# Kernel optimization log

Measured on AMD Instinct MI355X. Metric: run time of the kernel, lower is better.

The kernel has to match this reference:

```python
import jax, jax.numpy as jnp
import numpy as np


def _log_g(x):
    # log of g(x) = where(x>=0, x+0.5, sigmoid(x)), computed stably in log-space
    return jnp.where(x >= 0, jnp.log(jax.nn.relu(x) + 0.5), -jax.nn.softplus(-x))


def _mingru_layer(h, w_hg_l, w_out_l, rms_w_l):
    # h: [B,T,H]; w_hg_l: [2*DI,H]; w_out_l: [H,DI]; rms_w_l: [H]
    hg = jnp.einsum('bth,dh->btd', h, w_hg_l)          # [B,T,2*DI]
    hidden, gate = jnp.split(hg, 2, axis=-1)            # each [B,T,DI]
    log_coeffs = -jax.nn.softplus(gate)                 # log a_t
    log_values = -jax.nn.softplus(-gate) + _log_g(hidden)  # log(z_t * g(h~_t))
    # Heinsen log-space associative scan (prev_hidden = 0, contributes nothing)
    a_star = jnp.cumsum(log_coeffs, axis=1)
    log_h = a_star + jax.lax.cumlogsumexp(log_values - a_star, axis=1)
    out = jnp.exp(log_h)                                # [B,T,DI]
    out = jnp.einsum('btd,hd->bth', out, w_out_l) + h   # proj_out + residual
    eps = jnp.finfo(out.dtype).eps
    out = out * jax.lax.rsqrt(jnp.mean(out * out, axis=-1, keepdims=True) + eps)
    return out * rms_w_l


def setup_inputs() -> dict:
    key = jax.random.key(0)
    ks = jax.random.split(key, 6)
    B, T, OBS, H, DI, L, A = 32, 1024, 512, 512, 1024, 2, 16
    s = 0.05  # weight scale keeps softplus/exp chain well-conditioned
    return {
        'x': jax.random.normal(ks[0], (B, T, OBS), jnp.float32),
        'enc_w': s * jax.random.normal(ks[1], (H, OBS), jnp.float32),
        'enc_b': jnp.zeros((H,), jnp.float32),
        'w_hg': s * jax.random.normal(ks[2], (L, 2 * DI, H), jnp.float32),
        'w_out': s * jax.random.normal(ks[3], (L, H, DI), jnp.float32),
        'rms_w': jnp.ones((L, H), jnp.float32),
        'dec_w': s * jax.random.normal(ks[4], (A, H), jnp.float32),
        'dec_b': jnp.zeros((A,), jnp.float32),
        'val_w': s * jax.random.normal(ks[5], (1, H), jnp.float32),
        'val_b': jnp.zeros((1,), jnp.float32),
    }


def reference(x, enc_w, enc_b, w_hg, w_out, rms_w, dec_w, dec_b, val_w, val_b):
    B, T, _ = x.shape
    # encoder: Linear + exact gelu
    h = jax.nn.gelu(jnp.einsum('bto,ho->bth', x, enc_w) + enc_b, approximate=False)
    for l in range(w_hg.shape[0]):
        h = _mingru_layer(h, w_hg[l], w_out[l], rms_w[l])
    flat = h.reshape(B * T, -1)
    logits = flat @ dec_w.T + dec_b                     # [B*T, A]
    values = (flat @ val_w.T + val_b).reshape(B, T)
    return logits, values
```

## Files before the change

kernel.cpp:

```cpp
#include <hip/hip_runtime.h>
#include <math.h>

#define MROWS 32768
#define T_LEN 1024

typedef __attribute__((ext_vector_type(8))) short bf16x8;
typedef __attribute__((ext_vector_type(4))) float f32x4;

__device__ __forceinline__ unsigned short f2bf(float f) {
  union { float f; unsigned u; } x; x.f = f;
  unsigned r = x.u + 0x7fffu + ((x.u >> 16) & 1u);
  return (unsigned short)(r >> 16);
}
__device__ __forceinline__ float bf2f(unsigned short u) {
  union { unsigned u; float f; } x; x.u = ((unsigned)u) << 16; return x.f;
}

__device__ __forceinline__ void gload_lds16(const void* g, void* l) {
  __builtin_amdgcn_global_load_lds(
      (const __attribute__((address_space(1))) void*)g,
      (__attribute__((address_space(3))) void*)l, 16, 0, 0);
}

__device__ __forceinline__ float sigm_neg(float x) {
  return __builtin_amdgcn_rcpf(1.0f + __expf(x));
}

template<int MODE>
__global__ __launch_bounds__(256, 2)
void gemm_bt(const unsigned short* __restrict__ A, int lda,
             const unsigned short* __restrict__ B,
             int N, int K,
             const float* __restrict__ bias,
             const unsigned short* res,
             unsigned short* outb)
{
  __shared__ __align__(16) unsigned short sA[128 * 64];
  __shared__ __align__(16) unsigned short sB[128 * 64];
  const int tid  = threadIdx.x;
  const int wave = tid >> 6, lane = tid & 63;
  const int lid = blockIdx.x;
  const int swz = (lid & 7) * ((int)gridDim.x >> 3) + (lid >> 3);
  const int m0 = (swz >> 2) * 128;
  const int n0 = (swz & 3) * 128;
  const int srow   = lane >> 3;
  const int sslotb = ((lane & 7) ^ srow) * 16;
  const int wm = wave & 1, wn = wave >> 1;
  const int r16 = lane & 15, q = lane >> 4;

  f32x4 acc[4][4];
#pragma unroll
  for (int i = 0; i < 4; i++)
#pragma unroll
    for (int j = 0; j < 4; j++)
#pragma unroll
      for (int e = 0; e < 4; e++) acc[i][j][e] = 0.0f;

  const char* Ab = (const char*)A;
  const char* Bb = (const char*)B;
  char* sAb = (char*)sA;
  char* sBb = (char*)sB;

  for (int kt = 0; kt < K; kt += 64) {
#pragma unroll
    for (int i = 0; i < 4; i++) {
      const int j = wave * 4 + i;
      const int row = j * 8 + srow;
      gload_lds16(Ab + ((size_t)(m0 + row) * lda + kt) * 2 + sslotb, sAb + j * 1024);
      gload_lds16(Bb + ((size_t)(n0 + row) * K   + kt) * 2 + sslotb, sBb + j * 1024);
    }
    __syncthreads();
#pragma unroll
    for (int kh = 0; kh < 2; kh++) {
      bf16x8 af[4], bfr[4];
#pragma unroll
      for (int mt = 0; mt < 4; mt++) {
        const int row = wm * 64 + mt * 16 + r16;
        af[mt] = *(const bf16x8*)(sAb + row * 128 + ((((kh << 2) | q) ^ (row & 7)) * 16));
      }
#pragma unroll
      for (int nt = 0; nt < 4; nt++) {
        const int row = wn * 64 + nt * 16 + r16;
        bfr[nt] = *(const bf16x8*)(sBb + row * 128 + ((((kh << 2) | q) ^ (row & 7)) * 16));
      }
#pragma unroll
      for (int mt = 0; mt < 4; mt++)
#pragma unroll
        for (int nt = 0; nt < 4; nt++)
          acc[mt][nt] = __builtin_amdgcn_mfma_f32_16x16x32_bf16(af[mt], bfr[nt], acc[mt][nt], 0, 0, 0);
    }
    __syncthreads();
  }

#pragma unroll
  for (int mt = 0; mt < 4; mt++) {
#pragma unroll
    for (int nt = 0; nt < 4; nt++) {
#pragma unroll
      for (int r = 0; r < 4; r++) {
        const int m = m0 + wm * 64 + mt * 16 + q * 4 + r;
        const int n = n0 + wn * 64 + nt * 16 + r16;
        const size_t idx = (size_t)m * N + n;
        float v = acc[mt][nt][r];
        if (MODE == 0) {
          v += bias[n];
          v = 0.5f * v * (1.0f + erff(v * 0.70710678118654752f));
        } else if (MODE == 2) {
          v += bf2f(res[idx]);
        }
        outb[idx] = f2bf(v);
      }
    }
  }
}

__global__ __launch_bounds__(256, 2)
void gemm_hg(const unsigned short* __restrict__ A,
             const unsigned short* __restrict__ B,
             unsigned short* __restrict__ outb)
{
  __shared__ __align__(16) unsigned short sA [128 * 64];
  __shared__ __align__(16) unsigned short sB0[128 * 64];
  __shared__ __align__(16) unsigned short sB1[128 * 64];
  const int tid  = threadIdx.x;
  const int wave = tid >> 6, lane = tid & 63;
  const int lid = blockIdx.x;
  const int swz = (lid & 7) * 256 + (lid >> 3);
  const int m0  = (swz >> 3) * 128;
  const int nh0 = (swz & 7) * 128;
  const int srow   = lane >> 3;
  const int sslotb = ((lane & 7) ^ srow) * 16;
  const int wm = wave & 1, wn = wave >> 1;
  const int r16 = lane & 15, q = lane >> 4;

  f32x4 acc0[4][4], acc1[4][4];
#pragma unroll
  for (int i = 0; i < 4; i++)
#pragma unroll
    for (int j = 0; j < 4; j++)
#pragma unroll
      for (int e = 0; e < 4; e++) { acc0[i][j][e] = 0.0f; acc1[i][j][e] = 0.0f; }

  const char* Ab = (const char*)A;
  const char* Bb = (const char*)B;
  char* sAb  = (char*)sA;
  char* sB0b = (char*)sB0;
  char* sB1b = (char*)sB1;

  for (int kt = 0; kt < 512; kt += 64) {
#pragma unroll
    for (int i = 0; i < 4; i++) {
      const int j = wave * 4 + i;
      const int row = j * 8 + srow;
      gload_lds16(Ab + ((size_t)(m0 + row) * 512 + kt) * 2 + sslotb, sAb + j * 1024);
      gload_lds16(Bb + ((size_t)(nh0 + row) * 512 + kt) * 2 + sslotb, sB0b + j * 1024);
      gload_lds16(Bb + ((size_t)(1024 + nh0 + row) * 512 + kt) * 2 + sslotb, sB1b + j * 1024);
    }
    __syncthreads();
#pragma unroll
    for (int kh = 0; kh < 2; kh++) {
      bf16x8 af[4], b0r[4], b1r[4];
#pragma unroll
      for (int mt = 0; mt < 4; mt++) {
        const int row = wm * 64 + mt * 16 + r16;
        af[mt] = *(const bf16x8*)(sAb + row * 128 + ((((kh << 2) | q) ^ (row & 7)) * 16));
      }
#pragma unroll
      for (int nt = 0; nt < 4; nt++) {
        const int row = wn * 64 + nt * 16 + r16;
        const int so  = ((((kh << 2) | q) ^ (row & 7)) * 16);
        b0r[nt] = *(const bf16x8*)(sB0b + row * 128 + so);
        b1r[nt] = *(const bf16x8*)(sB1b + row * 128 + so);
      }
#pragma unroll
      for (int mt = 0; mt < 4; mt++)
#pragma unroll
        for (int nt = 0; nt < 4; nt++) {
          acc0[mt][nt] = __builtin_amdgcn_mfma_f32_16x16x32_bf16(af[mt], b0r[nt], acc0[mt][nt], 0, 0, 0);
          acc1[mt][nt] = __builtin_amdgcn_mfma_f32_16x16x32_bf16(af[mt], b1r[nt], acc1[mt][nt], 0, 0, 0);
        }
    }
    __syncthreads();
  }

#pragma unroll
  for (int mt = 0; mt < 4; mt++) {
#pragma unroll
    for (int nt = 0; nt < 4; nt++) {
#pragma unroll
      for (int r = 0; r < 4; r++) {
        const int m  = m0 + wm * 64 + mt * 16 + q * 4 + r;
        const int d  = nh0 + wn * 64 + nt * 16 + r16;
        const float vh = acc0[mt][nt][r];
        const float vg = acc1[mt][nt][r];
        const float G = (vh >= 0.0f) ? (vh + 0.5f) : sigm_neg(-vh);
        const float a = sigm_neg(vg);
        const float b = (1.0f - a) * G;
        const size_t base = (size_t)m * 2048 + d;
        outb[base]        = f2bf(b);
        outb[base + 1024] = f2bf(a);
      }
    }
  }
}

__global__ __launch_bounds__(256)
void scan_kernel(unsigned short* hg) {
  __shared__ unsigned long long sAB[256 * 16];
  __shared__ float sA[16 * 32];
  __shared__ float sH[16 * 32];
  const int b  = blockIdx.x >> 5;
  const int dg = blockIdx.x & 31;
  const int tid = threadIdx.x;
  const int c  = tid >> 4;
  const int dp = tid & 15;
  unsigned int* base = (unsigned int*)(hg + (size_t)b * T_LEN * 2048);
  const int du = dg * 16 + dp;

  float carry = 0.0f;

  for (int seg = 0; seg < 4; ++seg) {
    const int t0 = seg * 256 + c * 16;

    float A0 = 1.0f, A1 = 1.0f, h0 = 0.0f, h1 = 0.0f;
#pragma unroll
    for (int tl = 0; tl < 16; ++tl) {
      const int t = t0 + tl;
      const unsigned bpk = base[t * 1024 + du];
      const unsigned apk = base[t * 1024 + 512 + du];
      sAB[(c * 16 + tl) * 16 + dp] =
          (unsigned long long)apk | ((unsigned long long)bpk << 32);
      const float fa0 = bf2f((unsigned short)apk), fa1 = bf2f((unsigned short)(apk >> 16));
      const float fb0 = bf2f((unsigned short)bpk), fb1 = bf2f((unsigned short)(bpk >> 16));
      A0 *= fa0; h0 = fa0 * h0 + fb0;
      A1 *= fa1; h1 = fa1 * h1 + fb1;
    }
    sA[c * 32 + 2 * dp] = A0;  sA[c * 32 + 2 * dp + 1] = A1;
    sH[c * 32 + 2 * dp] = h0;  sH[c * 32 + 2 * dp + 1] = h1;
    __syncthreads();

    if (tid < 32) {
      float hin = carry;
#pragma unroll
      for (int cc = 0; cc < 16; ++cc) {
        const float a  = sA[cc * 32 + tid];
        const float hs = sH[cc * 32 + tid];
        sA[cc * 32 + tid] = hin;
        hin = hs + a * hin;
      }
      carry = hin;
    }
    __syncthreads();

    float hh0 = sA[c * 32 + 2 * dp];
    float hh1 = sA[c * 32 + 2 * dp + 1];
#pragma unroll
    for (int tl = 0; tl < 16; ++tl) {
      const int t = t0 + tl;
      const unsigned long long ab = sAB[(c * 16 + tl) * 16 + dp];
      const float fa0 = bf2f((unsigned short)ab);
      const float fa1 = bf2f((unsigned short)(ab >> 16));
      const float fb0 = bf2f((unsigned short)(ab >> 32));
      const float fb1 = bf2f((unsigned short)(ab >> 48));
      hh0 = fa0 * hh0 + fb0;
      hh1 = fa1 * hh1 + fb1;
      base[t * 1024 + 512 + du] = (unsigned)f2bf(hh0) | ((unsigned)f2bf(hh1) << 16);
    }
    __syncthreads();
  }
}

__global__ __launch_bounds__(256)
void rms_kernel(unsigned short* __restrict__ hb, const float* __restrict__ w) {
  const int wid  = (blockIdx.x * blockDim.x + threadIdx.x) >> 6;
  const int lane = threadIdx.x & 63;
  unsigned short* row = hb + (size_t)wid * 512;
  float v[8];
  float ss = 0.0f;
#pragma unroll
  for (int j = 0; j < 8; j++) { v[j] = bf2f(row[lane + 64 * j]); ss += v[j] * v[j]; }
#pragma unroll
  for (int off = 32; off >= 1; off >>= 1) ss += __shfl_xor(ss, off, 64);
  const float r = rsqrtf(ss * (1.0f / 512.0f) + 1.1920929e-7f);
#pragma unroll
  for (int j = 0; j < 8; j++) {
    const int k = lane + 64 * j;
    row[k] = f2bf(v[j] * r * w[k]);
  }
}

__global__ __launch_bounds__(256)
void rms_dec_kernel(const unsigned short* __restrict__ hb,
                    const float* __restrict__ w,
                    const float* __restrict__ dec_w,
                    const float* __restrict__ dec_b,
                    const float* __restrict__ val_w,
                    const float* __restrict__ val_b,
                    float* __restrict__ out) {
  const int row  = (blockIdx.x * blockDim.x + threadIdx.x) >> 6;
  const int lane = threadIdx.x & 63;
  const unsigned short* hr = hb + (size_t)row * 512;
  float v[8];
  float ss = 0.0f;
#pragma unroll
  for (int j = 0; j < 8; j++) { v[j] = bf2f(hr[lane + 64 * j]); ss += v[j] * v[j]; }
#pragma unroll
  for (int off = 32; off >= 1; off >>= 1) ss += __shfl_xor(ss, off, 64);
  const float r = rsqrtf(ss * (1.0f / 512.0f) + 1.1920929e-7f);

  float acc[17];
#pragma unroll
  for (int a = 0; a < 17; a++) acc[a] = 0.0f;
#pragma unroll
  for (int j = 0; j < 8; j++) {
    const int k = lane + 64 * j;
    const float hv = v[j] * r * w[k];
#pragma unroll
    for (int a = 0; a < 16; a++) acc[a] += hv * dec_w[a * 512 + k];
    acc[16] += hv * val_w[k];
  }
#pragma unroll
  for (int a = 0; a < 17; a++) {
#pragma unroll
    for (int off = 32; off >= 1; off >>= 1) acc[a] += __shfl_xor(acc[a], off, 64);
  }
  if (lane == 0) {
    float* logits = out;
    float* values = out + (size_t)MROWS * 16;
#pragma unroll
    for (int a = 0; a < 16; a++) logits[(size_t)row * 16 + a] = acc[a] + dec_b[a];
    values[row] = acc[16] + val_b[0];
  }
}

__global__ __launch_bounds__(256)
void conv_bf16(const float* __restrict__ in, unsigned short* __restrict__ out, int n4) {
  const int i = blockIdx.x * blockDim.x + threadIdx.x;
  if (i < n4) {
    const float4 v = ((const float4*)in)[i];
    const unsigned long long pack =
        (unsigned long long)f2bf(v.x) |
        ((unsigned long long)f2bf(v.y) << 16) |
        ((unsigned long long)f2bf(v.z) << 32) |
        ((unsigned long long)f2bf(v.w) << 48);
    ((unsigned long long*)out)[i] = pack;
  }
}

extern "C" void kernel_launch(void* const* d_in, const int* in_sizes, int n_in,
                              void* d_out, int out_size, void* d_ws, size_t ws_size,
                              hipStream_t stream) {
  const float* x     = (const float*)d_in[0];
  const float* enc_w = (const float*)d_in[1];
  const float* enc_b = (const float*)d_in[2];
  const float* w_hg  = (const float*)d_in[3];
  const float* w_out = (const float*)d_in[4];
  const float* rms_w = (const float*)d_in[5];
  const float* dec_w = (const float*)d_in[6];
  const float* dec_b = (const float*)d_in[7];
  const float* val_w = (const float*)d_in[8];
  const float* val_b = (const float*)d_in[9];
  float* out = (float*)d_out;

  if (ws_size < 174587904u) return;

  char* ws = (char*)d_ws;
  unsigned short* hg   = (unsigned short*)(ws);
  unsigned short* xb   = (unsigned short*)(ws);
  unsigned short* hb   = (unsigned short*)(ws + 134217728);
  unsigned short* wenc = (unsigned short*)(ws + 167772160);
  unsigned short* whg  = wenc + 262144;
  unsigned short* wout = whg + 2097152;

  conv_bf16<<<16384, 256, 0, stream>>>(x, xb, 4194304);
  conv_bf16<<<256,   256, 0, stream>>>(enc_w, wenc, 65536);
  conv_bf16<<<2048,  256, 0, stream>>>(w_hg, whg, 524288);
  conv_bf16<<<1024,  256, 0, stream>>>(w_out, wout, 262144);

  gemm_bt<0><<<1024, 256, 0, stream>>>(xb, 512, wenc, 512, 512, enc_b, nullptr, hb);

  for (int l = 0; l < 2; ++l) {
    gemm_hg<<<2048, 256, 0, stream>>>(hb, whg + (size_t)l * 1048576, hg);
    scan_kernel<<<1024, 256, 0, stream>>>(hg);
    gemm_bt<2><<<1024, 256, 0, stream>>>(hg + 1024, 2048, wout + (size_t)l * 524288,
                                         512, 1024, nullptr, hb, hb);
    if (l == 0) rms_kernel<<<8192, 256, 0, stream>>>(hb, rms_w);
  }

  rms_dec_kernel<<<8192, 256, 0, stream>>>(hb, rms_w + 512, dec_w, dec_b,
                                           val_w, val_b, out);
}
```

Baseline: 603.8 us.

## Rewrite hidden/gate GEMM with 256-row tiles and double-buffered async LDS pipeline

Replaces the 128x(2x128) hidden/gate GEMM with an 8-wave, 256-row tile kernel that uses a 128 KB double-buffered LDS ring. It streams the next K-step's global-to-LDS loads in quarters while computing on the current buffer, using explicit vmcnt/lgkmcnt waits, barriers and MFMA priority boosts. The aim is to hide global load latency and raise reuse of the weight tile per block. The cost is heavy LDS use (128 KB) and delicate hand-written synchronisation.

```diff
diff --git a/kernel.cpp b/kernel.cpp
--- a/kernel.cpp
+++ b/kernel.cpp
@@ -25,6 +25,12 @@
 __device__ __forceinline__ float sigm_neg(float x) {
   return __builtin_amdgcn_rcpf(1.0f + __expf(x));
 }
+
+#define VMCNT2 asm volatile("s_waitcnt vmcnt(2)" ::: "memory")
+#define VMCNT0 asm volatile("s_waitcnt vmcnt(0)" ::: "memory")
+#define LGKM0 do { asm volatile("s_waitcnt lgkmcnt(0)" ::: "memory"); \
+                   __builtin_amdgcn_sched_barrier(0); } while (0)
+#define BAR __builtin_amdgcn_s_barrier()
 
 template<int MODE>
 __global__ __launch_bounds__(256, 2)
@@ -114,85 +120,144 @@
   }
 }
 
-__global__ __launch_bounds__(256, 2)
-void gemm_hg(const unsigned short* __restrict__ A,
-             const unsigned short* __restrict__ B,
-             unsigned short* __restrict__ outb)
+__global__ __launch_bounds__(512, 2)
+void gemm_hg8(const unsigned short* __restrict__ A,
+              const unsigned short* __restrict__ B,
+              unsigned short* __restrict__ outb)
 {
-  __shared__ __align__(16) unsigned short sA [128 * 64];
-  __shared__ __align__(16) unsigned short sB0[128 * 64];
-  __shared__ __align__(16) unsigned short sB1[128 * 64];
+  __shared__ __align__(16) char smem[131072];
   const int tid  = threadIdx.x;
   const int wave = tid >> 6, lane = tid & 63;
   const int lid = blockIdx.x;
-  const int swz = (lid & 7) * 256 + (lid >> 3);
-  const int m0  = (swz >> 3) * 128;
+  const int swz = (lid & 7) * 128 + (lid >> 3);
+  const int m0  = (swz >> 3) * 256;
   const int nh0 = (swz & 7) * 128;
-  const int srow   = lane >> 3;
-  const int sslotb = ((lane & 7) ^ srow) * 16;
-  const int wm = wave & 1, wn = wave >> 1;
-  const int r16 = lane & 15, q = lane >> 4;
-
-  f32x4 acc0[4][4], acc1[4][4];
-#pragma unroll
-  for (int i = 0; i < 4; i++)
-#pragma unroll
-    for (int j = 0; j < 4; j++)
-#pragma unroll
-      for (int e = 0; e < 4; e++) { acc0[i][j][e] = 0.0f; acc1[i][j][e] = 0.0f; }
+  const int wm = wave >> 2, wn = wave & 3;
+  const int r16 = lane & 15, q4 = lane >> 4;
+
+  const int srow   = tid >> 3;
+  const int sslotb = ((tid & 7) ^ (srow & 7)) * 16;
+  const int sldso  = tid * 16;
+
+  const int slot0 = ((q4)     ^ (r16 & 7)) * 16;
+  const int slot1 = ((4 | q4) ^ (r16 & 7)) * 16;
 
   const char* Ab = (const char*)A;
   const char* Bb = (const char*)B;
-  char* sAb  = (char*)sA;
-  char* sB0b = (char*)sB0;
-  char* sB1b = (char*)sB1;
-
-  for (int kt = 0; kt < 512; kt += 64) {
-#pragma unroll
-    for (int i = 0; i < 4; i++) {
-      const int j = wave * 4 + i;
-      const int row = j * 8 + srow;
-      gload_lds16(Ab + ((size_t)(m0 + row) * 512 + kt) * 2 + sslotb, sAb + j * 1024);
-      gload_lds16(Bb + ((size_t)(nh0 + row) * 512 + kt) * 2 + sslotb, sB0b + j * 1024);
-      gload_lds16(Bb + ((size_t)(1024 + nh0 + row) * 512 + kt) * 2 + sslotb, sB1b + j * 1024);
-    }
-    __syncthreads();
-#pragma unroll
-    for (int kh = 0; kh < 2; kh++) {
-      bf16x8 af[4], b0r[4], b1r[4];
-#pragma unroll
-      for (int mt = 0; mt < 4; mt++) {
-        const int row = wm * 64 + mt * 16 + r16;
-        af[mt] = *(const bf16x8*)(sAb + row * 128 + ((((kh << 2) | q) ^ (row & 7)) * 16));
-      }
-#pragma unroll
-      for (int nt = 0; nt < 4; nt++) {
-        const int row = wn * 64 + nt * 16 + r16;
-        const int so  = ((((kh << 2) | q) ^ (row & 7)) * 16);
-        b0r[nt] = *(const bf16x8*)(sB0b + row * 128 + so);
-        b1r[nt] = *(const bf16x8*)(sB1b + row * 128 + so);
-      }
-#pragma unroll
-      for (int mt = 0; mt < 4; mt++)
-#pragma unroll
-        for (int nt = 0; nt < 4; nt++) {
-          acc0[mt][nt] = __builtin_amdgcn_mfma_f32_16x16x32_bf16(af[mt], b0r[nt], acc0[mt][nt], 0, 0, 0);
-          acc1[mt][nt] = __builtin_amdgcn_mfma_f32_16x16x32_bf16(af[mt], b1r[nt], acc1[mt][nt], 0, 0, 0);
-        }
-    }
-    __syncthreads();
-  }
-
-#pragma unroll
-  for (int mt = 0; mt < 4; mt++) {
-#pragma unroll
-    for (int nt = 0; nt < 4; nt++) {
-#pragma unroll
-      for (int r = 0; r < 4; r++) {
-        const int m  = m0 + wm * 64 + mt * 16 + q * 4 + r;
-        const int d  = nh0 + wn * 64 + nt * 16 + r16;
-        const float vh = acc0[mt][nt][r];
-        const float vg = acc1[mt][nt][r];
+
+  f32x4 acc[8][4];
+#pragma unroll
+  for (int i = 0; i < 8; i++)
+#pragma unroll
+    for (int j = 0; j < 4; j++)
+#pragma unroll
+      for (int e = 0; e < 4; e++) acc[i][j][e] = 0.0f;
+
+  auto stage2 = [&](int u, int qp) {
+    char* base = smem + (u & 1) * 65536;
+    const int kt2 = u << 7;
+#pragma unroll
+    for (int i = 0; i < 2; ++i) {
+      const int qq = qp * 2 + i;
+      if (qq < 4) {
+        gload_lds16(Ab + (size_t)(m0 + qq * 64 + srow) * 1024 + kt2 + sslotb,
+                    base + qq * 8192 + sldso);
+      } else if (qq < 6) {
+        gload_lds16(Bb + (size_t)(nh0 + (qq - 4) * 64 + srow) * 1024 + kt2 + sslotb,
+                    base + 32768 + (qq - 4) * 8192 + sldso);
+      } else {
+        gload_lds16(Bb + (size_t)(1024 + nh0 + (qq - 6) * 64 + srow) * 1024 + kt2 + sslotb,
+                    base + 49152 + (qq - 6) * 8192 + sldso);
+      }
+    }
+  };
+
+  auto lda_frags = [&](const char* base, int kh, int mh,
+                       bf16x8 af[4], bf16x8 bh[2], bf16x8 bg[2]) {
+    const int slot = kh ? slot1 : slot0;
+#pragma unroll
+    for (int mt = 0; mt < 4; ++mt) {
+      const int row = wm * 128 + mh * 64 + mt * 16 + r16;
+      af[mt] = *(const bf16x8*)(base + row * 128 + slot);
+    }
+#pragma unroll
+    for (int nt = 0; nt < 2; ++nt) {
+      const int row = wn * 32 + nt * 16 + r16;
+      bh[nt] = *(const bf16x8*)(base + 32768 + row * 128 + slot);
+      bg[nt] = *(const bf16x8*)(base + 49152 + row * 128 + slot);
+    }
+  };
+
+  auto mfma16 = [&](int mh, bf16x8 af[4], bf16x8 bh[2], bf16x8 bg[2]) {
+    __builtin_amdgcn_s_setprio(1);
+#pragma unroll
+    for (int mt = 0; mt < 4; ++mt) {
+      const int MT = mh * 4 + mt;
+      acc[MT][0] = __builtin_amdgcn_mfma_f32_16x16x32_bf16(af[mt], bh[0], acc[MT][0], 0, 0, 0);
+      acc[MT][1] = __builtin_amdgcn_mfma_f32_16x16x32_bf16(af[mt], bh[1], acc[MT][1], 0, 0, 0);
+      acc[MT][2] = __builtin_amdgcn_mfma_f32_16x16x32_bf16(af[mt], bg[0], acc[MT][2], 0, 0, 0);
+      acc[MT][3] = __builtin_amdgcn_mfma_f32_16x16x32_bf16(af[mt], bg[1], acc[MT][3], 0, 0, 0);
+    }
+    __builtin_amdgcn_s_setprio(0);
+  };
+
+#pragma unroll
+  for (int qp = 0; qp < 4; ++qp) stage2(0, qp);
+  VMCNT0; BAR;
+
+  for (int t = 0; t < 4; ++t) {
+    const int u1 = 2 * t + 1;
+    const char* b0 = smem;
+    const char* b1 = smem + 65536;
+    bf16x8 af[4], bh[2], bg[2];
+    const bool more = (t < 3);
+
+#pragma unroll
+    for (int pi = 0; pi < 4; ++pi) {
+      const int kh = pi >> 1, mh = pi & 1;
+      if (pi == 0) {
+        stage2(u1, 0);
+        VMCNT2;
+        BAR;
+        lda_frags(b0, kh, mh, af, bh, bg);
+      } else {
+        lda_frags(b0, kh, mh, af, bh, bg);
+        stage2(u1, pi);
+        BAR;
+      }
+      LGKM0;
+      mfma16(mh, af, bh, bg);
+      BAR;
+    }
+
+#pragma unroll
+    for (int pi = 0; pi < 4; ++pi) {
+      const int kh = pi >> 1, mh = pi & 1;
+      if (pi == 0) {
+        if (more) { stage2(u1 + 1, 0); VMCNT2; } else { VMCNT0; }
+        BAR;
+        lda_frags(b1, kh, mh, af, bh, bg);
+      } else {
+        lda_frags(b1, kh, mh, af, bh, bg);
+        if (more) stage2(u1 + 1, pi);
+        BAR;
+      }
+      LGKM0;
+      mfma16(mh, af, bh, bg);
+      BAR;
+    }
+  }
+
+#pragma unroll
+  for (int MT = 0; MT < 8; ++MT) {
+#pragma unroll
+    for (int nf = 0; nf < 2; ++nf) {
+#pragma unroll
+      for (int r = 0; r < 4; ++r) {
+        const int m = m0 + wm * 128 + MT * 16 + q4 * 4 + r;
+        const int d = nh0 + wn * 32 + nf * 16 + r16;
+        const float vh = acc[MT][nf][r];
+        const float vg = acc[MT][nf + 2][r];
         const float G = (vh >= 0.0f) ? (vh + 0.5f) : sigm_neg(-vh);
         const float a = sigm_neg(vg);
         const float b = (1.0f - a) * G;
@@ -380,7 +445,7 @@
   gemm_bt<0><<<1024, 256, 0, stream>>>(xb, 512, wenc, 512, 512, enc_b, nullptr, hb);
 
   for (int l = 0; l < 2; ++l) {
-    gemm_hg<<<2048, 256, 0, stream>>>(hb, whg + (size_t)l * 1048576, hg);
+    gemm_hg8<<<1024, 512, 0, stream>>>(hb, whg + (size_t)l * 1048576, hg);
     scan_kernel<<<1024, 256, 0, stream>>>(hg);
     gemm_bt<2><<<1024, 256, 0, stream>>>(hg + 1024, 2048, wout + (size_t)l * 524288,
                                          512, 1024, nullptr, hb, hb);
```

Result: faster. 572.5 us (-5.2%).
